# Optimization experiments

Measured on AMD Instinct MI355X. Metric: run time of the kernel, lower is better.

The kernel has to match this reference:

```python
import jax, jax.numpy as jnp
import numpy as np

N = 131072          # number of items ranked in one soft_rank call
CAPACITY = 3.0      # self.capcity in the torch module


def _pav_kl(y, w):
    """KL isotonic regression (non-increasing fit) via Pool-Adjacent-Violators.
    Pooled block value = logsumexp(y_block) - logsumexp(w_block).
    Matches torchsort / fast-soft-sort isotonic_kl. Sequential O(N)."""
    n = y.shape[0]

    def push(i, st):
        ly, lw, val, start, ptr = st
        ly = ly.at[ptr].set(y[i])
        lw = lw.at[ptr].set(w[i])
        val = val.at[ptr].set(y[i] - w[i])
        start = start.at[ptr].set(i)
        ptr = ptr + 1

        def cond(s):
            _, _, v, _, p = s
            return (p >= 2) & (v[p - 2] <= v[p - 1])

        def merge(s):
            ly, lw, v, stt, p = s
            ny = jnp.logaddexp(ly[p - 2], ly[p - 1])
            nw = jnp.logaddexp(lw[p - 2], lw[p - 1])
            return (ly.at[p - 2].set(ny), lw.at[p - 2].set(nw),
                    v.at[p - 2].set(ny - nw), stt, p - 1)

        return jax.lax.while_loop(cond, merge, (ly, lw, val, start, ptr))

    z = jnp.zeros((n,), y.dtype)
    st0 = (z, z, z, jnp.full((n,), n, jnp.int32), jnp.int32(0))
    ly, lw, val, start, ptr = jax.lax.fori_loop(0, n, push, st0)
    # invalidate stale stack slots, then map each element to its block value
    start = jnp.where(jnp.arange(n) < ptr, start, n)
    blk = jnp.searchsorted(start, jnp.arange(n), side='right') - 1
    return val[blk]


@jax.custom_vjp
def isotonic_kl(y, w):
    return _pav_kl(y, w)


def _iso_fwd(y, w):
    sol = _pav_kl(y, w)
    return sol, (y, w, sol)


def _iso_bwd(res, g):
    y, w, sol = res
    n = y.shape[0]
    # blocks = maximal runs of constant solution (exact equality by construction)
    blk = jnp.cumsum(jnp.concatenate([jnp.array([True]), sol[1:] != sol[:-1]])) - 1
    gsum = jax.ops.segment_sum(g, blk, num_segments=n)

    def seg_softmax(v):
        m = jax.ops.segment_max(v, blk, num_segments=n)
        lse = jnp.log(jax.ops.segment_sum(jnp.exp(v - m[blk]), blk, num_segments=n)) + m
        return jnp.exp(v - lse[blk])

    return seg_softmax(y) * gsum[blk], -seg_softmax(w) * gsum[blk]


isotonic_kl.defvjp(_iso_fwd, _iso_bwd)


def soft_rank_kl(scores):
    """torchsort.soft_rank(scores[None], regularization='kl'), strength=1, ascending."""
    n = scores.shape[0]
    w_log = jnp.log(jnp.arange(n, 0, -1, dtype=scores.dtype))  # log([n, ..., 1])
    perm = jnp.argsort(-scores)          # descending, stable
    s = scores[perm]
    sol = isotonic_kl(s, w_log)
    inv = jnp.argsort(perm)
    return jnp.exp(s - sol)[inv]


def setup_inputs() -> dict:
    key = jax.random.key(0)
    k = jax.random.split(key, 5)
    x = jax.random.normal(k[0], (N, 1), jnp.float32)
    # torch Linear default init bounds: 1/sqrt(fan_in)
    w1 = jax.random.uniform(k[1], (1, 32), jnp.float32, -1.0, 1.0)
    b1 = jax.random.uniform(k[2], (32,), jnp.float32, -1.0, 1.0)
    lim2 = 1.0 / np.sqrt(32.0)
    w2 = jax.random.uniform(k[3], (32, 1), jnp.float32, -lim2, lim2)
    b2 = jax.random.uniform(k[4], (1,), jnp.float32, -lim2, lim2)
    return {"x": x, "w1": w1, "b1": b1, "w2": w2, "b2": b2}


def reference(x, w1, b1, w2, b2):
    h = jnp.maximum(x @ w1 + b1, 0.0)            # [N, 32]
    scores = (h @ w2 + b2).reshape(-1)           # [N]
    ranks = soft_rank_kl(scores)                 # [N]
    other = jax.lax.stop_gradient(ranks) % CAPACITY
    ranks = (ranks - other) / CAPACITY + 1.0
    return ranks.reshape(-1, 1)
```

## Files before the change

kernel.cpp:

```cpp
#include <hip/hip_runtime.h>
#include <stdint.h>

typedef unsigned int u32;
typedef unsigned long long u64;

#define N_ITEMS 131072
#define NB 131072
#define NSLICE 4
#define NCHUNKS 2048
#define MBLK 64
#define BUCK_PER_BLK 2048
#define CH_PER_BLK 32
#define PAD 65
#define REGSLOT 2048
#define FIXSCALE 268435456.0f
#define FIXMASK ((1ull << 46) - 1)


__device__ __forceinline__ float wsumf(int s, int e) {
  return 0.5f * (float)(e - s + 1) * (float)(2 * N_ITEMS - s - e);
}

__device__ __forceinline__ float key_to_score(u32 key) {
  u32 m = ~key;
  u32 u = (m & 0x80000000u) ? (m ^ 0x80000000u) : ~m;
  return __uint_as_float(u);
}

#define LOG2E 1.4426950408889634f
__device__ __forceinline__ float fexp(float x) { return exp2f(x * LOG2E); }

__device__ __forceinline__ u32 bucket_of(u32 key, u32 kmin, u32 kmax) {
  double scale = (double)NB / ((double)(kmax - kmin) + 1.0);
  u32 b = (u32)((double)(key - kmin) * scale);
  return b < NB ? b : (NB - 1);
}

__device__ __forceinline__ float recSY(int2 r) { return __int_as_float(r.y); }


__global__ void score_key_kernel(const float* __restrict__ x,
                                 const float* __restrict__ w1,
                                 const float* __restrict__ b1,
                                 const float* __restrict__ w2,
                                 const float* __restrict__ b2,
                                 u32* __restrict__ keyRaw,
                                 u32* __restrict__ pmin, u32* __restrict__ pmax,
                                 u64* __restrict__ hist8, u64* __restrict__ flags) {
  __shared__ u32 r0[256], r1[256];
  int t = threadIdx.x;
  int i = blockIdx.x * 256 + t;
#pragma unroll
  for (int k = 0; k < NSLICE; ++k) hist8[(size_t)k * NB + i] = 0ull;
  if (i < MBLK) flags[i] = 0ull;
  float xv = x[i];
  float s = b2[0];
#pragma unroll
  for (int j = 0; j < 32; ++j) {
    float h = fmaf(xv, w1[j], b1[j]);
    h = fmaxf(h, 0.0f);
    s = fmaf(h, w2[j], s);
  }
  u32 u = __float_as_uint(s);
  u32 m = u ^ ((u & 0x80000000u) ? 0xFFFFFFFFu : 0x80000000u);
  u32 key = ~m;
  keyRaw[i] = key;
  r0[t] = key; r1[t] = key;
  __syncthreads();
  for (int off = 128; off > 0; off >>= 1) {
    if (t < off) { r0[t] = min(r0[t], r0[t + off]); r1[t] = max(r1[t], r1[t + off]); }
    __syncthreads();
  }
  if (t == 0) { pmin[blockIdx.x] = r0[0]; pmax[blockIdx.x] = r1[0]; }
}


__global__ void hist_kernel(const u32* __restrict__ keyRaw,
                            const u32* __restrict__ pmin, const u32* __restrict__ pmax,
                            u64* __restrict__ hist8, u32* __restrict__ mm) {
  __shared__ u32 s0[256], s1[256];
  int t = threadIdx.x;
  s0[t] = min(pmin[t], pmin[t + 256]);
  s1[t] = max(pmax[t], pmax[t + 256]);
  __syncthreads();
  for (int off = 128; off > 0; off >>= 1) {
    if (t < off) { s0[t] = min(s0[t], s0[t + off]); s1[t] = max(s1[t], s1[t + off]); }
    __syncthreads();
  }
  u32 kmin = s0[0], kmax = s1[0];
  if (blockIdx.x == 0 && t == 0) { mm[0] = kmin; mm[1] = kmax; }
  int i = blockIdx.x * 256 + t;
  u32 key = keyRaw[i];
  u32 g = bucket_of(key, kmin, kmax);
  float smax = key_to_score(kmin);
  float v = fexp(key_to_score(key) - smax);
  u64 fix = (u64)fmaxf(1.0f, fmaf(v, FIXSCALE, 0.5f));
  size_t slice = (size_t)(blockIdx.x & (NSLICE - 1)) * NB;
  atomicAdd(&hist8[slice + g], (1ull << 46) | fix);
}


__global__ __launch_bounds__(256) void scan_pav_merge_kernel(
    const u64* __restrict__ hist8, u64* __restrict__ flags,
    u32* __restrict__ cdf, int2* __restrict__ REC,
    int* __restrict__ cnt2, u32* __restrict__ rstart) {
  __shared__ u32 vals[BUCK_PER_BLK + 1];
  __shared__ float seL[BUCK_PER_BLK];
  __shared__ int   rST[CH_PER_BLK * PAD];
  __shared__ float rSY[CH_PER_BLK * PAD];
  __shared__ u32 sh[256];
  __shared__ u32 red64[64];
  __shared__ int lcnt[CH_PER_BLK];
  __shared__ int ca[16], cb[16], cM[16];
  int t = threadIdx.x, b = blockIdx.x;
  int B0 = b * BUCK_PER_BLK;
  for (int q = 0; q < 8; ++q) {
    int ii = q * 256 + t;
    u64 acc = 0;
#pragma unroll
    for (int c = 0; c < NSLICE; ++c) acc += hist8[(size_t)c * NB + B0 + ii];
    vals[ii] = (u32)(acc >> 46);
    seL[ii] = (float)(acc & FIXMASK) * (1.0f / FIXSCALE);
  }
  __syncthreads();
  u32 loc[8]; u32 s = 0;
  for (int q = 0; q < 8; ++q) { loc[q] = s; s += vals[t * 8 + q]; }
  sh[t] = s;
  __syncthreads();
  for (int off = 1; off < 256; off <<= 1) {
    u32 x2 = (t >= off) ? sh[t - off] : 0u;
    __syncthreads();
    sh[t] += x2;
    __syncthreads();
  }
  if (t == 0) atomicExch(&flags[b], (1ull << 32) | (u64)sh[255]);
  if (t < 64) {
    u32 v = 0;
    if (t < b) {
      u64 f;
      do { f = atomicAdd(&flags[t], 0ull); } while ((u32)(f >> 32) == 0u);
      v = (u32)f;
    }
    red64[t] = v;
  }
  __syncthreads();
  for (int off = 32; off > 0; off >>= 1) {
    if (t < off) red64[t] += red64[t + off];
    __syncthreads();
  }
  u32 exclu = red64[0];
  u32 tbase = ((t == 0) ? 0u : sh[t - 1]) + exclu;
  u32 eb8[8];
  for (int q = 0; q < 8; ++q) { eb8[q] = tbase + loc[q]; vals[t * 8 + q] = eb8[q]; }
  {
    uint4* c4 = (uint4*)(cdf + B0 + t * 8);
    c4[0] = make_uint4(eb8[0], eb8[1], eb8[2], eb8[3]);
    c4[1] = make_uint4(eb8[4], eb8[5], eb8[6], eb8[7]);
  }
  if (t == 255) vals[BUCK_PER_BLK] = exclu + sh[255];
  if (t == 0) rstart[b] = exclu;
  if (b == 0 && t == 0) rstart[MBLK] = N_ITEMS;
  __syncthreads();
  if (t < CH_PER_BLK) {
    int base = t * PAD;
    int ptr = 0; bool have = false;
    float syT = 0.0f; int stT = 0;
    for (int k = 0; k < 64; ++k) {
      u32 cs = vals[t * 64 + k], ce = vals[t * 64 + k + 1];
      if (ce == cs) continue;
      float syC = seL[t * 64 + k];
      int stC = (int)cs, eC = (int)ce - 1;
      while (have) {
        float SWc = wsumf(stC, eC);
        float SWt = wsumf(stT, stC - 1);
        if (!(syT * SWc <= syC * SWt)) break;
        syC += syT; stC = stT;
        if (ptr == 0) { have = false; break; }
        --ptr;
        stT = rST[base + ptr]; syT = rSY[base + ptr];
      }
      if (have) { rST[base + ptr] = stT; rSY[base + ptr] = syT; ++ptr; }
      stT = stC; syT = syC; have = true;
    }
    if (have) { rST[base + ptr] = stT; rSY[base + ptr] = syT; ++ptr; }
    lcnt[t] = ptr;
  }
  __syncthreads();
  for (int j = 0; j < 5; ++j) {
    int P = CH_PER_BLK >> (j + 1);
    if (t < P) {
      int p = t;
      int kL = p << (j + 1), kR = kL + (1 << j);
      int slotL = kL * PAD, slotR = kR * PAD;
      int nL = lcnt[kL], nR = lcnt[kR];
      int a = 0, bb = 0, hasM = 0;
      if (nL > 0 && nR > 0) {
        int gstartR = (int)vals[kR * 64];
        int gendR   = (int)vals[(kR + (1 << j)) * 64];
        float SYL = rSY[slotL + nL - 1]; int stL = rST[slotL + nL - 1];
        float SYR = rSY[slotR];
        int eR = (nR > 1) ? (rST[slotR + 1] - 1) : (gendR - 1);
        float SWL = wsumf(stL, gstartR - 1);
        float SWR = wsumf(gstartR, eR);
        if (SYL * SWR <= SYR * SWL) {
          hasM = 1;
          float SYM = SYL + SYR; int Ms = stL, Me = eR;
          a = 1; bb = 1;
          for (;;) {
            float SWM = wsumf(Ms, Me);
            if (a < nL) {
              float SYe = rSY[slotL + nL - 1 - a]; int ste = rST[slotL + nL - 1 - a];
              float SWe = wsumf(ste, Ms - 1);
              if (SYe * SWM <= SYM * SWe) { SYM += SYe; Ms = ste; ++a; continue; }
            }
            if (bb < nR) {
              float SYb = rSY[slotR + bb]; int sb = rST[slotR + bb];
              int eb = (bb + 1 < nR) ? (rST[slotR + bb + 1] - 1) : (gendR - 1);
              float SWb = wsumf(sb, eb);
              if (SYM * SWb <= SYb * SWM) { SYM += SYb; Me = eb; ++bb; continue; }
            }
            break;
          }
          rST[slotL + nL - a] = Ms; rSY[slotL + nL - a] = SYM;
        }
      }
      ca[p] = a; cb[p] = bb; cM[p] = hasM;
    }
    __syncthreads();
    for (int p = 0; p < P; ++p) {
      int kL = p << (j + 1), kR = kL + (1 << j);
      int nL = lcnt[kL], nR = lcnt[kR];
      int a = ca[p], bb = cb[p], hasM = cM[p];
      int slotL = kL * PAD, slotR = kR * PAD;
      int destBase = slotL + nL - a + hasM;
      int srcBase = slotR + bb;
      int ncopy = nR - bb;
      for (int off = 0; off < ncopy; off += blockDim.x) {
        int k2 = off + t; bool act = k2 < ncopy;
        int vt = 0; float vs = 0.f;
        if (act) { vt = rST[srcBase + k2]; vs = rSY[srcBase + k2]; }
        __syncthreads();
        if (act) { rST[destBase + k2] = vt; rSY[destBase + k2] = vs; }
        __syncthreads();
      }
    }
    __syncthreads();
    if (t < P) {
      int p = t; int kL = p << (j + 1), kR = kL + (1 << j);
      lcnt[kL] = lcnt[kL] - ca[p] + cM[p] + (lcnt[kR] - cb[p]);
    }
    __syncthreads();
  }
  int n = lcnt[0];
  for (int k = t; k < n; k += blockDim.x)
    REC[(size_t)b * REGSLOT + k] = make_int2(rST[k], __float_as_int(rSY[k]));
  if (t == 0) cnt2[b] = n;
}


__global__ void merge_region_kernel(int2* __restrict__ REC, int* __restrict__ cnt2,
                                    const u32* __restrict__ rstart, int l0, int L) {
  __shared__ int lcnt[8];
  __shared__ int ca[4], cb[4], cM[4];
  int t = threadIdx.x;
  int G = 1 << L;
  int SR = 1 << l0;
  int baseR = blockIdx.x * G * SR;
  if (t < G) lcnt[t] = cnt2[baseR + t * SR];
  __syncthreads();
  for (int j = 0; j < L; ++j) {
    int P = G >> (j + 1);
    if (t < P) {
      int p = t;
      int kL = p << (j + 1), kR = kL + (1 << j);
      int slotL = (baseR + kL * SR) * REGSLOT, slotR = (baseR + kR * SR) * REGSLOT;
      int nL = lcnt[kL], nR = lcnt[kR];
      int a = 0, bb = 0, hasM = 0;
      if (nL > 0 && nR > 0) {
        int gstartR = (int)rstart[baseR + kR * SR];
        int gendR   = (int)rstart[baseR + (kR + (1 << j)) * SR];
        int2 rL = REC[slotL + nL - 1];
        float SYL = recSY(rL); int stL = rL.x;
        int2 rR = REC[slotR];
        float SYR = recSY(rR);
        int eR = (nR > 1) ? (REC[slotR + 1].x - 1) : (gendR - 1);
        float SWL = wsumf(stL, gstartR - 1);
        float SWR = wsumf(gstartR, eR);
        if (SYL * SWR <= SYR * SWL) {
          hasM = 1;
          float SYM = SYL + SYR; int Ms = stL, Me = eR;
          a = 1; bb = 1;
          for (;;) {
            float SWM = wsumf(Ms, Me);
            if (a < nL) {
              int2 re = REC[slotL + nL - 1 - a];
              float SYe = recSY(re); int ste = re.x;
              float SWe = wsumf(ste, Ms - 1);
              if (SYe * SWM <= SYM * SWe) { SYM += SYe; Ms = ste; ++a; continue; }
            }
            if (bb < nR) {
              int2 rb = REC[slotR + bb];
              float SYb = recSY(rb); int sb = rb.x;
              int eb = (bb + 1 < nR) ? (REC[slotR + bb + 1].x - 1) : (gendR - 1);
              float SWb = wsumf(sb, eb);
              if (SYM * SWb <= SYb * SWM) { SYM += SYb; Me = eb; ++bb; continue; }
            }
            break;
          }
          REC[slotL + nL - a] = make_int2(Ms, __float_as_int(SYM));
        }
      }
      ca[p] = a; cb[p] = bb; cM[p] = hasM;
    }
    __syncthreads();
    for (int p = 0; p < P; ++p) {
      int kL = p << (j + 1), kR = kL + (1 << j);
      int nL = lcnt[kL], nR = lcnt[kR];
      int a = ca[p], bb = cb[p], hasM = cM[p];
      int slotL = (baseR + kL * SR) * REGSLOT, slotR = (baseR + kR * SR) * REGSLOT;
      int destBase = slotL + nL - a + hasM;
      int srcBase = slotR + bb;
      int ncopy = nR - bb;
      for (int off = 0; off < ncopy; off += blockDim.x) {
        int k2 = off + t; bool act = k2 < ncopy;
        int2 vr = make_int2(0, 0);
        if (act) vr = REC[srcBase + k2];
        __syncthreads();
        if (act) REC[destBase + k2] = vr;
        __syncthreads();
      }
    }
    __syncthreads();
    if (t < P) {
      int p = t; int kL = p << (j + 1), kR = kL + (1 << j);
      lcnt[kL] = lcnt[kL] - ca[p] + cM[p] + (lcnt[kR] - cb[p]);
    }
    __syncthreads();
  }
  if (t == 0) cnt2[baseR] = lcnt[0];
}


__global__ void out_kernel(const u32* __restrict__ keyRaw, const u32* __restrict__ mm,
                           const u32* __restrict__ cdf,
                           const int2* __restrict__ REC,
                           const int* __restrict__ cnt2, float* __restrict__ out) {
  int i = blockIdx.x * 256 + threadIdx.x;
  u32 key = keyRaw[i];
  u32 kmin = mm[0], kmax = mm[1];
  float smax = key_to_score(kmin);
  u32 g = bucket_of(key, kmin, kmax);
  int p = (int)cdf[g];
  int m = cnt2[0];
  int lo = 0, hi = m - 1;
  while (lo < hi) {
    int mid = (lo + hi + 1) >> 1;
    if (REC[mid].x <= p) lo = mid; else hi = mid - 1;
  }
  int2 r = REC[lo];
  int s0 = r.x;
  int e0 = (lo + 1 < m) ? (REC[lo + 1].x - 1) : (N_ITEMS - 1);
  float SW = wsumf(s0, e0);
  float s = key_to_score(key);
  float rank = fexp(s - smax) * SW / recSY(r);
  out[i] = floorf(rank * (1.0f / 3.0f)) + 1.0f;
}


extern "C" void kernel_launch(void* const* d_in, const int* in_sizes, int n_in,
                              void* d_out, int out_size, void* d_ws, size_t ws_size,
                              hipStream_t stream) {
  const float* x  = (const float*)d_in[0];
  const float* w1 = (const float*)d_in[1];
  const float* b1 = (const float*)d_in[2];
  const float* w2 = (const float*)d_in[3];
  const float* b2 = (const float*)d_in[4];
  float* out = (float*)d_out;

  char* ws = (char*)d_ws;
  size_t o = 0;
  u32* mm     = (u32*)(ws + o); o += 16;
  u32* pmin   = (u32*)(ws + o); o += (size_t)512 * 4;
  u32* pmax   = (u32*)(ws + o); o += (size_t)512 * 4;
  u64* hist8  = (u64*)(ws + o); o += (size_t)NSLICE * NB * 8;
  u64* flags  = (u64*)(ws + o); o += (size_t)MBLK * 8;
  u32* cdf    = (u32*)(ws + o); o += (size_t)(NB + 4) * 4;
  u32* rstart = (u32*)(ws + o); o += (size_t)(MBLK + 4) * 4;
  u32* keyRaw = (u32*)(ws + o); o += (size_t)N_ITEMS * 4;
  int2* REC   = (int2*)(ws + o); o += (size_t)N_ITEMS * 8;
  int* cnt2   = (int*)(ws + o);  o += (size_t)MBLK * 4;

  score_key_kernel<<<512, 256, 0, stream>>>(x, w1, b1, w2, b2,
                                            keyRaw, pmin, pmax, hist8, flags);
  hist_kernel<<<512, 256, 0, stream>>>(keyRaw, pmin, pmax, hist8, mm);
  scan_pav_merge_kernel<<<MBLK, 256, 0, stream>>>(hist8, flags, cdf, REC, cnt2, rstart);
  merge_region_kernel<<<8, 256, 0, stream>>>(REC, cnt2, rstart, 0, 3);
  merge_region_kernel<<<1, 1024, 0, stream>>>(REC, cnt2, rstart, 3, 3);
  out_kernel<<<512, 256, 0, stream>>>(keyRaw, mm, cdf, REC, cnt2, out);
}
```

Baseline: 114.8 us.

## Fuse pipeline into two persistent kernels with grid-wide spin barriers

Merges score and histogram kernels using an atomic grid barrier for the global min/max, and folds the region merge tree and output pass into the scan/PAV kernel via inter-block flag handoff in a binary-tree merge. Zeroing moves to a single hipMemsetAsync. The in-block record copy is made per-wavefront without block-wide syncs, and the final lookup uses LDS when the record list fits. The intent is to remove several kernel launches and their serialization. The cost is that spin barriers assume all 512 and 64 blocks are co-resident, and many blocks sit idle waiting during the serial merge levels.

```diff
diff --git a/kernel.cpp b/kernel.cpp
--- a/kernel.cpp
+++ b/kernel.cpp
@@ -7,7 +7,6 @@
 #define N_ITEMS 131072
 #define NB 131072
 #define NSLICE 4
-#define NCHUNKS 2048
 #define MBLK 64
 #define BUCK_PER_BLK 2048
 #define CH_PER_BLK 32
@@ -39,20 +38,15 @@
 __device__ __forceinline__ float recSY(int2 r) { return __int_as_float(r.y); }
 
 
-__global__ void score_key_kernel(const float* __restrict__ x,
-                                 const float* __restrict__ w1,
-                                 const float* __restrict__ b1,
-                                 const float* __restrict__ w2,
-                                 const float* __restrict__ b2,
-                                 u32* __restrict__ keyRaw,
-                                 u32* __restrict__ pmin, u32* __restrict__ pmax,
-                                 u64* __restrict__ hist8, u64* __restrict__ flags) {
+__global__ __launch_bounds__(256) void score_hist_kernel(
+    const float* __restrict__ x,
+    const float* __restrict__ w1, const float* __restrict__ b1,
+    const float* __restrict__ w2, const float* __restrict__ b2,
+    u32* __restrict__ keyRaw, u32* __restrict__ pmin, u32* __restrict__ pmax,
+    u32* __restrict__ done, u64* __restrict__ hist8, u32* __restrict__ mm) {
   __shared__ u32 r0[256], r1[256];
   int t = threadIdx.x;
   int i = blockIdx.x * 256 + t;
-#pragma unroll
-  for (int k = 0; k < NSLICE; ++k) hist8[(size_t)k * NB + i] = 0ull;
-  if (i < MBLK) flags[i] = 0ull;
   float xv = x[i];
   float s = b2[0];
 #pragma unroll
@@ -71,26 +65,24 @@
     if (t < off) { r0[t] = min(r0[t], r0[t + off]); r1[t] = max(r1[t], r1[t + off]); }
     __syncthreads();
   }
-  if (t == 0) { pmin[blockIdx.x] = r0[0]; pmax[blockIdx.x] = r1[0]; }
-}
-
-
-__global__ void hist_kernel(const u32* __restrict__ keyRaw,
-                            const u32* __restrict__ pmin, const u32* __restrict__ pmax,
-                            u64* __restrict__ hist8, u32* __restrict__ mm) {
-  __shared__ u32 s0[256], s1[256];
-  int t = threadIdx.x;
-  s0[t] = min(pmin[t], pmin[t + 256]);
-  s1[t] = max(pmax[t], pmax[t + 256]);
+  if (t == 0) {
+    pmin[blockIdx.x] = r0[0];
+    pmax[blockIdx.x] = r1[0];
+    __threadfence();
+    atomicAdd(done, 1u);
+    while (atomicAdd(done, 0u) < 512u) __builtin_amdgcn_s_sleep(2);
+  }
+  __syncthreads();
+  __threadfence();
+  r0[t] = min(pmin[t], pmin[t + 256]);
+  r1[t] = max(pmax[t], pmax[t + 256]);
   __syncthreads();
   for (int off = 128; off > 0; off >>= 1) {
-    if (t < off) { s0[t] = min(s0[t], s0[t + off]); s1[t] = max(s1[t], s1[t + off]); }
-    __syncthreads();
-  }
-  u32 kmin = s0[0], kmax = s1[0];
+    if (t < off) { r0[t] = min(r0[t], r0[t + off]); r1[t] = max(r1[t], r1[t + off]); }
+    __syncthreads();
+  }
+  u32 kmin = r0[0], kmax = r1[0];
   if (blockIdx.x == 0 && t == 0) { mm[0] = kmin; mm[1] = kmax; }
-  int i = blockIdx.x * 256 + t;
-  u32 key = keyRaw[i];
   u32 g = bucket_of(key, kmin, kmax);
   float smax = key_to_score(kmin);
   float v = fexp(key_to_score(key) - smax);
@@ -100,18 +92,21 @@
 }
 
 
-__global__ __launch_bounds__(256) void scan_pav_merge_kernel(
-    const u64* __restrict__ hist8, u64* __restrict__ flags,
+__global__ __launch_bounds__(256) void solve_kernel(
+    const u64* __restrict__ hist8, u64* __restrict__ flags, u64* __restrict__ flag2,
     u32* __restrict__ cdf, int2* __restrict__ REC,
-    int* __restrict__ cnt2, u32* __restrict__ rstart) {
+    const u32* __restrict__ keyRaw, const u32* __restrict__ mm,
+    float* __restrict__ out) {
   __shared__ u32 vals[BUCK_PER_BLK + 1];
   __shared__ float seL[BUCK_PER_BLK];
   __shared__ int   rST[CH_PER_BLK * PAD];
   __shared__ float rSY[CH_PER_BLK * PAD];
   __shared__ u32 sh[256];
-  __shared__ u32 red64[64];
+  __shared__ u32 agg[64];
+  __shared__ u32 regS[65];
   __shared__ int lcnt[CH_PER_BLK];
   __shared__ int ca[16], cb[16], cM[16];
+  __shared__ int shInt[4];
   int t = threadIdx.x, b = blockIdx.x;
   int B0 = b * BUCK_PER_BLK;
   for (int q = 0; q < 8; ++q) {
@@ -135,20 +130,23 @@
   }
   if (t == 0) atomicExch(&flags[b], (1ull << 32) | (u64)sh[255]);
   if (t < 64) {
-    u32 v = 0;
-    if (t < b) {
-      u64 f;
-      do { f = atomicAdd(&flags[t], 0ull); } while ((u32)(f >> 32) == 0u);
-      v = (u32)f;
-    }
-    red64[t] = v;
-  }
-  __syncthreads();
-  for (int off = 32; off > 0; off >>= 1) {
-    if (t < off) red64[t] += red64[t + off];
-    __syncthreads();
-  }
-  u32 exclu = red64[0];
+    u64 f;
+    do { f = atomicAdd(&flags[t], 0ull); } while ((u32)(f >> 32) == 0u);
+    agg[t] = (u32)f;
+  }
+  __syncthreads();
+  if (t < 64) {
+    u32 v = agg[t];
+    u32 inc = v;
+    for (int off = 1; off < 64; off <<= 1) {
+      u32 o2 = __shfl_up(inc, off);
+      if (t >= off) inc += o2;
+    }
+    regS[t] = inc - v;
+    if (t == 63) regS[64] = inc;
+  }
+  __syncthreads();
+  u32 exclu = regS[b];
   u32 tbase = ((t == 0) ? 0u : sh[t - 1]) + exclu;
   u32 eb8[8];
   for (int q = 0; q < 8; ++q) { eb8[q] = tbase + loc[q]; vals[t * 8 + q] = eb8[q]; }
@@ -158,8 +156,6 @@
     c4[1] = make_uint4(eb8[4], eb8[5], eb8[6], eb8[7]);
   }
   if (t == 255) vals[BUCK_PER_BLK] = exclu + sh[255];
-  if (t == 0) rstart[b] = exclu;
-  if (b == 0 && t == 0) rstart[MBLK] = N_ITEMS;
   __syncthreads();
   if (t < CH_PER_BLK) {
     int base = t * PAD;
@@ -227,21 +223,21 @@
       ca[p] = a; cb[p] = bb; cM[p] = hasM;
     }
     __syncthreads();
-    for (int p = 0; p < P; ++p) {
-      int kL = p << (j + 1), kR = kL + (1 << j);
-      int nL = lcnt[kL], nR = lcnt[kR];
-      int a = ca[p], bb = cb[p], hasM = cM[p];
-      int slotL = kL * PAD, slotR = kR * PAD;
-      int destBase = slotL + nL - a + hasM;
-      int srcBase = slotR + bb;
-      int ncopy = nR - bb;
-      for (int off = 0; off < ncopy; off += blockDim.x) {
-        int k2 = off + t; bool act = k2 < ncopy;
-        int vt = 0; float vs = 0.f;
-        if (act) { vt = rST[srcBase + k2]; vs = rSY[srcBase + k2]; }
-        __syncthreads();
-        if (act) { rST[destBase + k2] = vt; rSY[destBase + k2] = vs; }
-        __syncthreads();
+    {
+      int w = t >> 6, lane = t & 63;
+      for (int p = w; p < P; p += 4) {
+        int kL = p << (j + 1), kR = kL + (1 << j);
+        int nL = lcnt[kL], nR = lcnt[kR];
+        int a = ca[p], bb = cb[p], hasM = cM[p];
+        int destBase = kL * PAD + nL - a + hasM;
+        int srcBase = kR * PAD + bb;
+        int ncopy = nR - bb;
+        for (int off = 0; off < ncopy; off += 64) {
+          int k2 = off + lane; bool act = k2 < ncopy;
+          int vt = 0; float vs = 0.f;
+          if (act) { vt = rST[srcBase + k2]; vs = rSY[srcBase + k2]; }
+          if (act) { rST[destBase + k2] = vt; rSY[destBase + k2] = vs; }
+        }
       }
     }
     __syncthreads();
@@ -251,34 +247,38 @@
     }
     __syncthreads();
   }
-  int n = lcnt[0];
-  for (int k = t; k < n; k += blockDim.x)
+  int myCnt = lcnt[0];
+  for (int k = t; k < myCnt; k += 256)
     REC[(size_t)b * REGSLOT + k] = make_int2(rST[k], __float_as_int(rSY[k]));
-  if (t == 0) cnt2[b] = n;
-}
-
-
-__global__ void merge_region_kernel(int2* __restrict__ REC, int* __restrict__ cnt2,
-                                    const u32* __restrict__ rstart, int l0, int L) {
-  __shared__ int lcnt[8];
-  __shared__ int ca[4], cb[4], cM[4];
-  int t = threadIdx.x;
-  int G = 1 << L;
-  int SR = 1 << l0;
-  int baseR = blockIdx.x * G * SR;
-  if (t < G) lcnt[t] = cnt2[baseR + t * SR];
-  __syncthreads();
-  for (int j = 0; j < L; ++j) {
-    int P = G >> (j + 1);
-    if (t < P) {
-      int p = t;
-      int kL = p << (j + 1), kR = kL + (1 << j);
-      int slotL = (baseR + kL * SR) * REGSLOT, slotR = (baseR + kR * SR) * REGSLOT;
-      int nL = lcnt[kL], nR = lcnt[kR];
+  __syncthreads();
+  int lvl = 0;
+  for (;;) {
+    if (b & (1 << lvl)) {
+      __threadfence();
+      if (t == 0) atomicExch(&flag2[b], (1ull << 32) | (u64)(u32)myCnt);
+      break;
+    }
+    if (lvl == 6) {
+      __threadfence();
+      if (t == 0) atomicExch(&flag2[0], (2ull << 32) | (u64)(u32)myCnt);
+      break;
+    }
+    int pb = b + (1 << lvl);
+    if (t == 0) {
+      u64 f;
+      do { f = atomicAdd(&flag2[pb], 0ull); __builtin_amdgcn_s_sleep(1); } while ((f >> 32) == 0ull);
+      shInt[0] = (int)(u32)f;
+    }
+    __syncthreads();
+    __threadfence();
+    int nR = shInt[0];
+    int nL = myCnt;
+    int slotL = b * REGSLOT, slotR = pb * REGSLOT;
+    if (t == 0) {
       int a = 0, bb = 0, hasM = 0;
       if (nL > 0 && nR > 0) {
-        int gstartR = (int)rstart[baseR + kR * SR];
-        int gendR   = (int)rstart[baseR + (kR + (1 << j)) * SR];
+        int gstartR = (int)regS[pb];
+        int gendR   = (int)regS[b + (2 << lvl)];
         int2 rL = REC[slotL + nL - 1];
         float SYL = recSY(rL); int stL = rL.x;
         int2 rR = REC[slotR];
@@ -310,60 +310,74 @@
           REC[slotL + nL - a] = make_int2(Ms, __float_as_int(SYM));
         }
       }
-      ca[p] = a; cb[p] = bb; cM[p] = hasM;
-    }
-    __syncthreads();
-    for (int p = 0; p < P; ++p) {
-      int kL = p << (j + 1), kR = kL + (1 << j);
-      int nL = lcnt[kL], nR = lcnt[kR];
-      int a = ca[p], bb = cb[p], hasM = cM[p];
-      int slotL = (baseR + kL * SR) * REGSLOT, slotR = (baseR + kR * SR) * REGSLOT;
-      int destBase = slotL + nL - a + hasM;
-      int srcBase = slotR + bb;
-      int ncopy = nR - bb;
-      for (int off = 0; off < ncopy; off += blockDim.x) {
-        int k2 = off + t; bool act = k2 < ncopy;
-        int2 vr = make_int2(0, 0);
-        if (act) vr = REC[srcBase + k2];
-        __syncthreads();
-        if (act) REC[destBase + k2] = vr;
-        __syncthreads();
-      }
-    }
-    __syncthreads();
-    if (t < P) {
-      int p = t; int kL = p << (j + 1), kR = kL + (1 << j);
-      lcnt[kL] = lcnt[kL] - ca[p] + cM[p] + (lcnt[kR] - cb[p]);
-    }
-    __syncthreads();
-  }
-  if (t == 0) cnt2[baseR] = lcnt[0];
-}
-
-
-__global__ void out_kernel(const u32* __restrict__ keyRaw, const u32* __restrict__ mm,
-                           const u32* __restrict__ cdf,
-                           const int2* __restrict__ REC,
-                           const int* __restrict__ cnt2, float* __restrict__ out) {
-  int i = blockIdx.x * 256 + threadIdx.x;
-  u32 key = keyRaw[i];
+      shInt[1] = a; shInt[2] = bb; shInt[3] = hasM;
+    }
+    __syncthreads();
+    int a = shInt[1], bb = shInt[2], hasM = shInt[3];
+    int destBase = slotL + nL - a + hasM;
+    int srcBase = slotR + bb;
+    int ncopy = nR - bb;
+    for (int off = 0; off < ncopy; off += 256) {
+      int k2 = off + t; bool act = k2 < ncopy;
+      int2 vr = make_int2(0, 0);
+      if (act) vr = REC[srcBase + k2];
+      __syncthreads();
+      if (act) REC[destBase + k2] = vr;
+      __syncthreads();
+    }
+    __syncthreads();
+    myCnt = nL - a + hasM + (nR - bb);
+    ++lvl;
+  }
+  if (t == 0) {
+    u64 f;
+    do { f = atomicAdd(&flag2[0], 0ull); __builtin_amdgcn_s_sleep(2); } while ((f >> 32) != 2ull);
+    shInt[0] = (int)(u32)f;
+  }
+  __syncthreads();
+  __threadfence();
+  int m = shInt[0];
+  bool useL = (m <= CH_PER_BLK * PAD);
+  if (useL) {
+    for (int k = t; k < m; k += 256) {
+      int2 r = REC[k];
+      rST[k] = r.x; rSY[k] = __int_as_float(r.y);
+    }
+  }
+  __syncthreads();
   u32 kmin = mm[0], kmax = mm[1];
   float smax = key_to_score(kmin);
-  u32 g = bucket_of(key, kmin, kmax);
-  int p = (int)cdf[g];
-  int m = cnt2[0];
-  int lo = 0, hi = m - 1;
-  while (lo < hi) {
-    int mid = (lo + hi + 1) >> 1;
-    if (REC[mid].x <= p) lo = mid; else hi = mid - 1;
-  }
-  int2 r = REC[lo];
-  int s0 = r.x;
-  int e0 = (lo + 1 < m) ? (REC[lo + 1].x - 1) : (N_ITEMS - 1);
-  float SW = wsumf(s0, e0);
-  float s = key_to_score(key);
-  float rank = fexp(s - smax) * SW / recSY(r);
-  out[i] = floorf(rank * (1.0f / 3.0f)) + 1.0f;
+  for (int q = 0; q < 8; ++q) {
+    int i = b * 2048 + q * 256 + t;
+    u32 key = keyRaw[i];
+    u32 g = bucket_of(key, kmin, kmax);
+    int p = (int)cdf[g];
+    int lo = 0, hi = m - 1;
+    if (useL) {
+      while (lo < hi) {
+        int mid = (lo + hi + 1) >> 1;
+        if (rST[mid] <= p) lo = mid; else hi = mid - 1;
+      }
+      int s0 = rST[lo];
+      int e0 = (lo + 1 < m) ? (rST[lo + 1] - 1) : (N_ITEMS - 1);
+      float SW = wsumf(s0, e0);
+      float sc = key_to_score(key);
+      float rank = fexp(sc - smax) * SW / rSY[lo];
+      out[i] = floorf(rank * (1.0f / 3.0f)) + 1.0f;
+    } else {
+      while (lo < hi) {
+        int mid = (lo + hi + 1) >> 1;
+        if (REC[mid].x <= p) lo = mid; else hi = mid - 1;
+      }
+      int2 r = REC[lo];
+      int s0 = r.x;
+      int e0 = (lo + 1 < m) ? (REC[lo + 1].x - 1) : (N_ITEMS - 1);
+      float SW = wsumf(s0, e0);
+      float sc = key_to_score(key);
+      float rank = fexp(sc - smax) * SW / recSY(r);
+      out[i] = floorf(rank * (1.0f / 3.0f)) + 1.0f;
+    }
+  }
 }
 
 
@@ -382,19 +396,18 @@
   u32* mm     = (u32*)(ws + o); o += 16;
   u32* pmin   = (u32*)(ws + o); o += (size_t)512 * 4;
   u32* pmax   = (u32*)(ws + o); o += (size_t)512 * 4;
+  u32* cdf    = (u32*)(ws + o); o += (size_t)(NB + 4) * 4;
+  u32* keyRaw = (u32*)(ws + o); o += (size_t)N_ITEMS * 4;
+  int2* REC   = (int2*)(ws + o); o += (size_t)N_ITEMS * 8;
+  char* zbase = ws + o;
   u64* hist8  = (u64*)(ws + o); o += (size_t)NSLICE * NB * 8;
   u64* flags  = (u64*)(ws + o); o += (size_t)MBLK * 8;
-  u32* cdf    = (u32*)(ws + o); o += (size_t)(NB + 4) * 4;
-  u32* rstart = (u32*)(ws + o); o += (size_t)(MBLK + 4) * 4;
-  u32* keyRaw = (u32*)(ws + o); o += (size_t)N_ITEMS * 4;
-  int2* REC   = (int2*)(ws + o); o += (size_t)N_ITEMS * 8;
-  int* cnt2   = (int*)(ws + o);  o += (size_t)MBLK * 4;
-
-  score_key_kernel<<<512, 256, 0, stream>>>(x, w1, b1, w2, b2,
-                                            keyRaw, pmin, pmax, hist8, flags);
-  hist_kernel<<<512, 256, 0, stream>>>(keyRaw, pmin, pmax, hist8, mm);
-  scan_pav_merge_kernel<<<MBLK, 256, 0, stream>>>(hist8, flags, cdf, REC, cnt2, rstart);
-  merge_region_kernel<<<8, 256, 0, stream>>>(REC, cnt2, rstart, 0, 3);
-  merge_region_kernel<<<1, 1024, 0, stream>>>(REC, cnt2, rstart, 3, 3);
-  out_kernel<<<512, 256, 0, stream>>>(keyRaw, mm, cdf, REC, cnt2, out);
-}
+  u64* flag2  = (u64*)(ws + o); o += (size_t)MBLK * 8;
+  u32* done   = (u32*)(ws + o); o += 64;
+  size_t zbytes = (size_t)((ws + o) - zbase);
+
+  hipMemsetAsync(zbase, 0, zbytes, stream);
+  score_hist_kernel<<<512, 256, 0, stream>>>(x, w1, b1, w2, b2,
+                                             keyRaw, pmin, pmax, done, hist8, mm);
+  solve_kernel<<<MBLK, 256, 0, stream>>>(hist8, flags, flag2, cdf, REC, keyRaw, mm, out);
+}
```

New measurement: 184.4 us. 1.61x slower.
